# Optimization experiments

Hardware: AMD Instinct MI355X
Metric: run time of the kernel (lower is better)

## Reference

```python
import jax, jax.numpy as jnp
import numpy as np

# SplineConv (PyG), dim=1, kernel_size=2, degree=1, open spline, aggr='mean',
# root_weight=True, bias=True.
# For K=2, m=1, dim=1 the B-spline basis per edge reduces exactly to
#   basis = (1 - u, u) with kernel indices (0, 1), u = edge_attr[:, 0] in [0, 1].

N_NODES = 50000
N_EDGES = 1600000
D_IN = 128
D_OUT = 128


def setup_inputs() -> dict:
    key = jax.random.key(0)
    k1, k2, k3, k4, k5, k6, k7 = jax.random.split(key, 7)
    x = jax.random.normal(k1, (N_NODES, D_IN), dtype=jnp.float32)
    edge_index = jax.random.randint(k2, (2, N_EDGES), 0, N_NODES, dtype=jnp.int64)
    edge_attr = jax.random.uniform(k3, (N_EDGES, 1), dtype=jnp.float32)
    # Glorot-ish init for spline weights [K^dim=2, D_IN, D_OUT]
    scale = 1.0 / np.sqrt(D_IN)
    W = jax.random.normal(k4, (2, D_IN, D_OUT), dtype=jnp.float32) * scale
    W_root = jax.random.normal(k5, (D_IN, D_OUT), dtype=jnp.float32) * scale
    bias = jax.random.normal(k6, (D_OUT,), dtype=jnp.float32) * 0.01
    return {"x": x, "edge_index": edge_index, "edge_attr": edge_attr,
            "W": W, "W_root": W_root, "bias": bias}


def reference(x, edge_index, edge_attr, W, W_root, bias):
    n = x.shape[0]
    src, dst = edge_index[0], edge_index[1]
    u = jnp.clip(edge_attr[:, 0], 0.0, 1.0)          # [E]
    # Node-level GEMMs for both kernel weight slots (cheaper than per-edge GEMM)
    h = jnp.einsum('nd,kde->kne', x, W)              # [2, N, D_OUT]
    # Per-edge spline-weighted message: (1-u)*h0[src] + u*h1[src]
    msg = (1.0 - u)[:, None] * h[0][src] + u[:, None] * h[1][src]  # [E, D_OUT]
    agg = jax.ops.segment_sum(msg, dst, num_segments=n)            # [N, D_OUT]
    deg = jax.ops.segment_sum(jnp.ones_like(u), dst, num_segments=n)
    agg = agg / jnp.maximum(deg, 1.0)[:, None]       # mean aggregation
    return agg + x @ W_root + bias
```

## Files before the change

### kernel.cpp

```cpp
#include <hip/hip_runtime.h>

static constexpr int N = 50000;
static constexpr int E = 1600000;
static constexpr int D = 128;
static constexpr int NB = (N + 63) / 64;
static constexpr int BIN_BLKS = 256;
static constexpr int CHUNK = E / BIN_BLKS;
static constexpr int SLOTS = (CHUNK + 1023) / 1024;
static constexpr int BKT_CAP = 3072;
static constexpr int CVT_BLKS = (N * D / 8 + 1023) / 1024;
static constexpr int W_BLKS = 48;

typedef __attribute__((ext_vector_type(8))) short short8;
typedef __attribute__((ext_vector_type(4))) float f32x4;
typedef __attribute__((ext_vector_type(2))) float f32x2;

__device__ __forceinline__ uint bf16rne2(float a, float b) {
    uint ua = __float_as_uint(a), ub = __float_as_uint(b);
    ua += 0x7fffu + ((ua >> 16) & 1u);
    ub += 0x7fffu + ((ub >> 16) & 1u);
    return (ua >> 16) | (ub & 0xffff0000u);
}

__device__ __forceinline__ int logical_blk() {
    return (blockIdx.x & 7) * (BIN_BLKS / 8) + (blockIdx.x >> 3);
}

__global__ __launch_bounds__(1024) void binprep_k(
        const int* __restrict__ ei, const float* __restrict__ ea,
        const float* __restrict__ x, const float* __restrict__ W,
        const float* __restrict__ Wr, int* __restrict__ gcur,
        uint* __restrict__ pay, ushort* __restrict__ xb,
        uchar* __restrict__ xf8, ushort* __restrict__ Wt) {
    __shared__ int hist[NB];
    __shared__ int pfx[NB];
    __shared__ int base[NB];
    __shared__ uint srtpay[CHUNK];
    __shared__ int  srtpos[CHUNK];
    __shared__ int wsum[16];
    __shared__ int tot_s;
    int t = threadIdx.x;
    int lane = t & 63, wv = t >> 6;
    if (blockIdx.x < BIN_BLKS) {
        int b = logical_blk();
        if (t < NB) hist[t] = 0;
        __syncthreads();
        int b0 = b * CHUNK;
        uint mypay[SLOTS];
        int  mybkt[SLOTS];
        int  myrank[SLOTS];
#pragma unroll
        for (int k = 0; k < SLOTS; ++k) {
            int i = b0 + t + k * 1024;
            myrank[k] = -1;
            if (t + k * 1024 < CHUNK) {
                int dst = ei[E + i];
                if ((unsigned)dst < (unsigned)N) {
                    int src = ei[i];
                    float u = fminf(fmaxf(ea[i], 0.0f), 1.0f);
                    uint u10 = (uint)(u * 1023.0f + 0.5f);
                    int bkt = dst >> 6;
                    mybkt[k] = bkt;
                    mypay[k] = (u10 << 22) | ((uint)(dst & 63) << 16) | (uint)src;
                    myrank[k] = atomicAdd(&hist[bkt], 1);
                }
            }
        }
        __syncthreads();
        int c = (t < NB) ? hist[t] : 0;
        int s = c;
#pragma unroll
        for (int d = 1; d < 64; d <<= 1) {
            int o = __shfl_up(s, d);
            if (lane >= d) s += o;
        }
        if (lane == 63) wsum[wv] = s;
        __syncthreads();
        if (t < 16) {
            int v = wsum[t];
            int si = v;
#pragma unroll
            for (int d = 1; d < 16; d <<= 1) {
                int o = __shfl_up(si, d);
                if (t >= d) si += o;
            }
            wsum[t] = si - v;
            if (t == 15) tot_s = si;
        }
        __syncthreads();
        int excl = s - c + wsum[wv];
        if (t < NB) {
            pfx[t] = excl;
            base[t] = c ? atomicAdd(&gcur[t], c) : 0;
        }
        __syncthreads();
#pragma unroll
        for (int k = 0; k < SLOTS; ++k) {
            if (myrank[k] >= 0) {
                int bk = mybkt[k];
                int slot = pfx[bk] + myrank[k];
                srtpay[slot] = mypay[k];
                int p = base[bk] + myrank[k];
                srtpos[slot] = (p < BKT_CAP) ? (bk * BKT_CAP + p) : -1;
            }
        }
        __syncthreads();
        int tot = tot_s;
        for (int i = t; i < tot; i += 1024) {
            int pos = srtpos[i];
            if (pos >= 0) pay[pos] = srtpay[i];
        }
    } else if (blockIdx.x < BIN_BLKS + CVT_BLKS) {
        int i = (blockIdx.x - BIN_BLKS) * 1024 + t;
        if (i < N * D / 8) {
            float4 v0 = ((const float4*)x)[2 * i];
            float4 v1 = ((const float4*)x)[2 * i + 1];
            uint4 ob = { bf16rne2(v0.x, v0.y), bf16rne2(v0.z, v0.w),
                         bf16rne2(v1.x, v1.y), bf16rne2(v1.z, v1.w) };
            ((uint4*)xb)[i] = ob;
            int lo = __builtin_amdgcn_cvt_pk_fp8_f32(v0.x, v0.y, 0, false);
            lo = __builtin_amdgcn_cvt_pk_fp8_f32(v0.z, v0.w, lo, true);
            int hi = __builtin_amdgcn_cvt_pk_fp8_f32(v1.x, v1.y, 0, false);
            hi = __builtin_amdgcn_cvt_pk_fp8_f32(v1.z, v1.w, hi, true);
            uint2 o8 = { (uint)lo, (uint)hi };
            ((uint2*)xf8)[i] = o8;
        }
    } else {
        int i = (blockIdx.x - BIN_BLKS - CVT_BLKS) * 1024 + t;
        int n = i / 384, r = i % 384;
        float v = (r < 256) ? W[(size_t)r * 128 + n]
                            : Wr[(size_t)(r - 256) * 128 + n];
        uint u = __float_as_uint(v);
        u += 0x7fffu + ((u >> 16) & 1u);
        Wt[(size_t)n * 384 + r] = (ushort)(u >> 16);
    }
}

__global__ __launch_bounds__(1024) void sortagg_k(
        const uchar* __restrict__ xf8, const int* __restrict__ gcur,
        const uint* __restrict__ pay, ushort* __restrict__ a0b,
        ushort* __restrict__ a1b) {
    __shared__ uint srt[BKT_CAP];
    __shared__ int hist[64];
    __shared__ int off64[65];
    int b = blockIdx.x, t = threadIdx.x;
    int beg = b * BKT_CAP;
    int c = gcur[b];
    if (c > BKT_CAP) c = BKT_CAP;
    if (t < 64) hist[t] = 0;
    __syncthreads();
    uint mypay[3]; int myrank[3];
#pragma unroll
    for (int k = 0; k < 3; ++k) {
        int i = t + k * 1024;
        if (i < c) {
            uint p = pay[beg + i];
            mypay[k] = p;
            myrank[k] = atomicAdd(&hist[(p >> 16) & 63], 1);
        }
    }
    __syncthreads();
    if (t < 64) {
        int v = hist[t];
        int s = v;
        for (int d = 1; d < 64; d <<= 1) {
            int o = __shfl_up(s, d);
            if (t >= d) s += o;
        }
        off64[t] = s - v;
        if (t == 63) off64[64] = s;
    }
    __syncthreads();
#pragma unroll
    for (int k = 0; k < 3; ++k) {
        int i = t + k * 1024;
        if (i < c) {
            uint p = mypay[k];
            srt[off64[(p >> 16) & 63] + myrank[k]] = p;
        }
    }
    __syncthreads();

    int lane = t & 63;
    int wv   = t >> 6;
    int grp  = (lane >> 4);
    int cl   = lane & 15;
    int nloc = wv * 4 + grp;
    int s0 = off64[nloc], s1 = off64[nloc + 1];
    int deg = s1 - s0;

    f32x2 S[4], T[4];
#pragma unroll
    for (int q = 0; q < 4; ++q) { S[q] = 0.f; T[q] = 0.f; }

    int j = s0;
    for (; j + 3 < s1; j += 4) {
        uint p[4];
        uint2 v[4];
#pragma unroll
        for (int d = 0; d < 4; ++d) p[d] = srt[j + d];
#pragma unroll
        for (int d = 0; d < 4; ++d)
            v[d] = *(const uint2*)(xf8 + (size_t)(p[d] & 0xffffu) * D + cl * 8);
#pragma unroll
        for (int d = 0; d < 4; ++d) {
            float u = (float)(p[d] >> 22) * (1.0f / 1023.0f);
            f32x2 u2 = {u, u};
            f32x2 xv0 = __builtin_amdgcn_cvt_pk_f32_fp8((int)v[d].x, false);
            f32x2 xv1 = __builtin_amdgcn_cvt_pk_f32_fp8((int)v[d].x, true);
            f32x2 xv2 = __builtin_amdgcn_cvt_pk_f32_fp8((int)v[d].y, false);
            f32x2 xv3 = __builtin_amdgcn_cvt_pk_f32_fp8((int)v[d].y, true);
            S[0] += xv0; T[0] = u2 * xv0 + T[0];
            S[1] += xv1; T[1] = u2 * xv1 + T[1];
            S[2] += xv2; T[2] = u2 * xv2 + T[2];
            S[3] += xv3; T[3] = u2 * xv3 + T[3];
        }
    }
    for (; j < s1; ++j) {
        uint p0 = srt[j];
        uint2 v0 = *(const uint2*)(xf8 + (size_t)(p0 & 0xffffu) * D + cl * 8);
        float u = (float)(p0 >> 22) * (1.0f / 1023.0f);
        f32x2 u2 = {u, u};
        f32x2 xv0 = __builtin_amdgcn_cvt_pk_f32_fp8((int)v0.x, false);
        f32x2 xv1 = __builtin_amdgcn_cvt_pk_f32_fp8((int)v0.x, true);
        f32x2 xv2 = __builtin_amdgcn_cvt_pk_f32_fp8((int)v0.y, false);
        f32x2 xv3 = __builtin_amdgcn_cvt_pk_f32_fp8((int)v0.y, true);
        S[0] += xv0; T[0] = u2 * xv0 + T[0];
        S[1] += xv1; T[1] = u2 * xv1 + T[1];
        S[2] += xv2; T[2] = u2 * xv2 + T[2];
        S[3] += xv3; T[3] = u2 * xv3 + T[3];
    }

    int node = b * 64 + nloc;
    if (node < N) {
        float inv = 1.0f / fmaxf((float)deg, 1.0f);
        uint4 oa = { bf16rne2((S[0].x - T[0].x) * inv, (S[0].y - T[0].y) * inv),
                     bf16rne2((S[1].x - T[1].x) * inv, (S[1].y - T[1].y) * inv),
                     bf16rne2((S[2].x - T[2].x) * inv, (S[2].y - T[2].y) * inv),
                     bf16rne2((S[3].x - T[3].x) * inv, (S[3].y - T[3].y) * inv) };
        uint4 ob = { bf16rne2(T[0].x * inv, T[0].y * inv),
                     bf16rne2(T[1].x * inv, T[1].y * inv),
                     bf16rne2(T[2].x * inv, T[2].y * inv),
                     bf16rne2(T[3].x * inv, T[3].y * inv) };
        *(uint4*)(a0b + (size_t)node * D + cl * 8) = oa;
        *(uint4*)(a1b + (size_t)node * D + cl * 8) = ob;
    }
}

__global__ __launch_bounds__(256) void gemm_k(
        const ushort* __restrict__ a0b, const ushort* __restrict__ a1b,
        const ushort* __restrict__ xb, const ushort* __restrict__ Wt,
        const float* __restrict__ bias, float* __restrict__ out) {
    int t    = threadIdx.x;
    int lane = t & 63;
    int w    = t >> 6;
    int r2   = w >> 1, c2 = w & 1;
    int q    = lane >> 4;
    int l16  = lane & 15;
    int row0 = blockIdx.x * 128;

    f32x4 acc[4][4];
#pragma unroll
    for (int i = 0; i < 4; ++i)
#pragma unroll
        for (int j = 0; j < 4; ++j) acc[i][j] = 0.f;

    const ushort* Asrc[3] = {a0b, a1b, xb};

    int arow[4];
#pragma unroll
    for (int mt = 0; mt < 4; ++mt) {
        int r = row0 + r2 * 64 + mt * 16 + l16;
        arow[mt] = r < N ? r : N - 1;
    }

#pragma unroll
    for (int kt = 0; kt < 384; kt += 32) {
        const ushort* Ab = Asrc[kt >> 7];
        int ko = (kt & 127) + q * 8;
        short8 af[4], bf[4];
#pragma unroll
        for (int mt = 0; mt < 4; ++mt)
            af[mt] = *(const short8*)(Ab + (size_t)arow[mt] * 128 + ko);
#pragma unroll
        for (int nt = 0; nt < 4; ++nt) {
            int n = c2 * 64 + nt * 16 + l16;
            bf[nt] = *(const short8*)(Wt + (size_t)n * 384 + kt + q * 8);
        }
#pragma unroll
        for (int mt = 0; mt < 4; ++mt)
#pragma unroll
            for (int nt = 0; nt < 4; ++nt)
                acc[mt][nt] = __builtin_amdgcn_mfma_f32_16x16x32_bf16(
                    af[mt], bf[nt], acc[mt][nt], 0, 0, 0);
    }

#pragma unroll
    for (int nt = 0; nt < 4; ++nt) {
        int col = c2 * 64 + nt * 16 + l16;
        float bb = bias[col];
#pragma unroll
        for (int mt = 0; mt < 4; ++mt) {
#pragma unroll
            for (int r = 0; r < 4; ++r) {
                int row = row0 + r2 * 64 + mt * 16 + q * 4 + r;
                if (row < N) out[(size_t)row * 128 + col] = acc[mt][nt][r] + bb;
            }
        }
    }
}

extern "C" void kernel_launch(void* const* d_in, const int* in_sizes, int n_in,
                              void* d_out, int out_size, void* d_ws, size_t ws_size,
                              hipStream_t stream) {
    const float* x    = (const float*)d_in[0];
    const int*   ei   = (const int*)d_in[1];
    const float* ea   = (const float*)d_in[2];
    const float* W    = (const float*)d_in[3];
    const float* Wr   = (const float*)d_in[4];
    const float* bias = (const float*)d_in[5];
    float* out = (float*)d_out;

    char* ws = (char*)d_ws;
    size_t o = 0;
    auto alloc = [&](size_t bytes) -> void* {
        void* p = ws + o;
        o = (o + bytes + 255) & ~(size_t)255;
        return p;
    };
    int*    gcur = (int*)alloc((size_t)NB * 4);
    uint*   pay  = (uint*)alloc((size_t)NB * BKT_CAP * 4);
    ushort* xb   = (ushort*)alloc((size_t)N * D * 2);
    uchar*  xf8  = (uchar*)alloc((size_t)N * D);
    ushort* a0b  = (ushort*)alloc((size_t)N * D * 2);
    ushort* a1b  = (ushort*)alloc((size_t)N * D * 2);
    ushort* Wt   = (ushort*)alloc((size_t)128 * 384 * 2);
    (void)ws_size; (void)in_sizes; (void)n_in; (void)out_size;

    hipMemsetAsync(gcur, 0, (size_t)NB * 4, stream);
    binprep_k<<<BIN_BLKS + CVT_BLKS + W_BLKS, 1024, 0, stream>>>(
                 ei, ea, x, W, Wr, gcur, pay, xb, xf8, Wt);
    sortagg_k<<<NB, 1024, 0, stream>>>(xf8, gcur, pay, a0b, a1b);
    gemm_k   <<<(N + 127) / 128, 256, 0, stream>>>(a0b, a1b, xb, Wt, bias, out);
}
```

Measured before the change: 171.2 us.

## Stage GEMM A/B tiles in LDS via direct global-to-LDS loads with XOR swizzle

The final GEMM kernel now stages 128x64 tiles of A and B into shared memory using global_load_lds (direct global-to-LDS copies) with an XOR-swizzled layout, instead of each wave loading its MFMA operands straight from global memory. This is meant to cut redundant global/L2 traffic, since operands are now shared across the waves in a block, and to avoid LDS bank conflicts. In exchange it adds two barriers per K-step and has no double buffering, so load latency is not overlapped with compute. The GEMM is only a part of the total pipeline.

Measured after the change: 159.1 us. -7.1%, faster.

```diff
diff --git a/kernel.cpp b/kernel.cpp
--- a/kernel.cpp
+++ b/kernel.cpp
@@ -20,6 +20,12 @@
     ua += 0x7fffu + ((ua >> 16) & 1u);
     ub += 0x7fffu + ((ub >> 16) & 1u);
     return (ua >> 16) | (ub & 0xffff0000u);
+}
+
+__device__ __forceinline__ void gload16(const void* g, void* l) {
+    __builtin_amdgcn_global_load_lds(
+        (const __attribute__((address_space(1))) void*)g,
+        (__attribute__((address_space(3))) void*)l, 16, 0, 0);
 }
 
 __device__ __forceinline__ int logical_blk() {
@@ -251,6 +257,9 @@
         const ushort* __restrict__ a0b, const ushort* __restrict__ a1b,
         const ushort* __restrict__ xb, const ushort* __restrict__ Wt,
         const float* __restrict__ bias, float* __restrict__ out) {
+    __shared__ ushort As[128 * 64];
+    __shared__ ushort Bs[128 * 64];
+
     int t    = threadIdx.x;
     int lane = t & 63;
     int w    = t >> 6;
@@ -258,6 +267,9 @@
     int q    = lane >> 4;
     int l16  = lane & 15;
     int row0 = blockIdx.x * 128;
+    int rsub  = lane >> 3;
+    int cslot = lane & 7;
+    int xorc  = cslot ^ rsub;
 
     f32x4 acc[4][4];
 #pragma unroll
@@ -267,32 +279,42 @@
 
     const ushort* Asrc[3] = {a0b, a1b, xb};
 
-    int arow[4];
-#pragma unroll
-    for (int mt = 0; mt < 4; ++mt) {
-        int r = row0 + r2 * 64 + mt * 16 + l16;
-        arow[mt] = r < N ? r : N - 1;
-    }
-
-#pragma unroll
-    for (int kt = 0; kt < 384; kt += 32) {
+#pragma unroll
+    for (int kt = 0; kt < 384; kt += 64) {
         const ushort* Ab = Asrc[kt >> 7];
-        int ko = (kt & 127) + q * 8;
-        short8 af[4], bf[4];
-#pragma unroll
-        for (int mt = 0; mt < 4; ++mt)
-            af[mt] = *(const short8*)(Ab + (size_t)arow[mt] * 128 + ko);
-#pragma unroll
-        for (int nt = 0; nt < 4; ++nt) {
-            int n = c2 * 64 + nt * 16 + l16;
-            bf[nt] = *(const short8*)(Wt + (size_t)n * 384 + kt + q * 8);
-        }
-#pragma unroll
-        for (int mt = 0; mt < 4; ++mt)
-#pragma unroll
-            for (int nt = 0; nt < 4; ++nt)
-                acc[mt][nt] = __builtin_amdgcn_mfma_f32_16x16x32_bf16(
-                    af[mt], bf[nt], acc[mt][nt], 0, 0, 0);
+        int ko = kt & 127;
+#pragma unroll
+        for (int h = 0; h < 4; ++h) {
+            int region = h * 4 + w;
+            int r = region * 8 + rsub;
+            int ra = row0 + r; ra = ra < N ? ra : N - 1;
+            gload16(Ab + (size_t)ra * 128 + ko + xorc * 8, As + region * 512);
+            gload16(Wt + (size_t)r * 384 + kt + xorc * 8,  Bs + region * 512);
+        }
+        __syncthreads();
+#pragma unroll
+        for (int kk = 0; kk < 2; ++kk) {
+            short8 af[4], bf[4];
+#pragma unroll
+            for (int mt = 0; mt < 4; ++mt) {
+                int r = r2 * 64 + mt * 16 + l16;
+                int slot = (kk * 4 + q) ^ (r & 7);
+                af[mt] = *(const short8*)&As[r * 64 + slot * 8];
+            }
+#pragma unroll
+            for (int nt = 0; nt < 4; ++nt) {
+                int n = c2 * 64 + nt * 16 + l16;
+                int slot = (kk * 4 + q) ^ (n & 7);
+                bf[nt] = *(const short8*)&Bs[n * 64 + slot * 8];
+            }
+#pragma unroll
+            for (int mt = 0; mt < 4; ++mt)
+#pragma unroll
+                for (int nt = 0; nt < 4; ++nt)
+                    acc[mt][nt] = __builtin_amdgcn_mfma_f32_16x16x32_bf16(
+                        af[mt], bf[nt], acc[mt][nt], 0, 0, 0);
+        }
+        __syncthreads();
     }
 
 #pragma unroll
```

## Fuse aggregation and output GEMM into one kernel via shared-memory tiles

Applied to the files above, without the earlier changes.

Merges the sort/aggregate kernel with the GEMM kernel. Each 64-node block now writes its mean-aggregated bf16 rows into XOR-swizzled shared memory and then runs MFMA over them plus the x rows. This drops the global a0b/a1b intermediates and one kernel launch. In exchange each block adds 32KB of shared memory, which may lower occupancy, and uses a smaller per-wave GEMM tile with more redundant loads of Wt.

Result: slower. 192.3 us (+12.3%).

```diff
diff --git a/kernel.cpp b/kernel.cpp
--- a/kernel.cpp
+++ b/kernel.cpp
@@ -136,13 +136,16 @@
     }
 }
 
-__global__ __launch_bounds__(1024) void sortagg_k(
+__global__ __launch_bounds__(1024) void sortagggemm_k(
         const uchar* __restrict__ xf8, const int* __restrict__ gcur,
-        const uint* __restrict__ pay, ushort* __restrict__ a0b,
-        ushort* __restrict__ a1b) {
+        const uint* __restrict__ pay, const ushort* __restrict__ xb,
+        const ushort* __restrict__ Wt, const float* __restrict__ bias,
+        float* __restrict__ out) {
     __shared__ uint srt[BKT_CAP];
     __shared__ int hist[64];
     __shared__ int off64[65];
+    __shared__ ushort A0[64 * 128];
+    __shared__ ushort A1[64 * 128];
     int b = blockIdx.x, t = threadIdx.x;
     int beg = b * BKT_CAP;
     int c = gcur[b];
@@ -231,8 +234,7 @@
         S[3] += xv3; T[3] = u2 * xv3 + T[3];
     }
 
-    int node = b * 64 + nloc;
-    if (node < N) {
+    {
         float inv = 1.0f / fmaxf((float)deg, 1.0f);
         uint4 oa = { bf16rne2((S[0].x - T[0].x) * inv, (S[0].y - T[0].y) * inv),
                      bf16rne2((S[1].x - T[1].x) * inv, (S[1].y - T[1].y) * inv),
@@ -242,70 +244,46 @@
                      bf16rne2(T[1].x * inv, T[1].y * inv),
                      bf16rne2(T[2].x * inv, T[2].y * inv),
                      bf16rne2(T[3].x * inv, T[3].y * inv) };
-        *(uint4*)(a0b + (size_t)node * D + cl * 8) = oa;
-        *(uint4*)(a1b + (size_t)node * D + cl * 8) = ob;
-    }
-}
-
-__global__ __launch_bounds__(256) void gemm_k(
-        const ushort* __restrict__ a0b, const ushort* __restrict__ a1b,
-        const ushort* __restrict__ xb, const ushort* __restrict__ Wt,
-        const float* __restrict__ bias, float* __restrict__ out) {
-    int t    = threadIdx.x;
-    int lane = t & 63;
-    int w    = t >> 6;
-    int r2   = w >> 1, c2 = w & 1;
-    int q    = lane >> 4;
-    int l16  = lane & 15;
-    int row0 = blockIdx.x * 128;
-
-    f32x4 acc[4][4];
-#pragma unroll
-    for (int i = 0; i < 4; ++i)
-#pragma unroll
-        for (int j = 0; j < 4; ++j) acc[i][j] = 0.f;
-
-    const ushort* Asrc[3] = {a0b, a1b, xb};
-
-    int arow[4];
-#pragma unroll
-    for (int mt = 0; mt < 4; ++mt) {
-        int r = row0 + r2 * 64 + mt * 16 + l16;
-        arow[mt] = r < N ? r : N - 1;
-    }
-
-#pragma unroll
-    for (int kt = 0; kt < 384; kt += 32) {
-        const ushort* Ab = Asrc[kt >> 7];
-        int ko = (kt & 127) + q * 8;
-        short8 af[4], bf[4];
-#pragma unroll
-        for (int mt = 0; mt < 4; ++mt)
-            af[mt] = *(const short8*)(Ab + (size_t)arow[mt] * 128 + ko);
-#pragma unroll
-        for (int nt = 0; nt < 4; ++nt) {
-            int n = c2 * 64 + nt * 16 + l16;
-            bf[nt] = *(const short8*)(Wt + (size_t)n * 384 + kt + q * 8);
-        }
-#pragma unroll
-        for (int mt = 0; mt < 4; ++mt)
-#pragma unroll
-            for (int nt = 0; nt < 4; ++nt)
-                acc[mt][nt] = __builtin_amdgcn_mfma_f32_16x16x32_bf16(
-                    af[mt], bf[nt], acc[mt][nt], 0, 0, 0);
-    }
-
-#pragma unroll
-    for (int nt = 0; nt < 4; ++nt) {
-        int col = c2 * 64 + nt * 16 + l16;
-        float bb = bias[col];
-#pragma unroll
-        for (int mt = 0; mt < 4; ++mt) {
-#pragma unroll
-            for (int r = 0; r < 4; ++r) {
-                int row = row0 + r2 * 64 + mt * 16 + q * 4 + r;
-                if (row < N) out[(size_t)row * 128 + col] = acc[mt][nt][r] + bb;
-            }
+        int pc = cl ^ (nloc & 7);
+        *(uint4*)&A0[nloc * 128 + pc * 8] = oa;
+        *(uint4*)&A1[nloc * 128 + pc * 8] = ob;
+    }
+    __syncthreads();
+
+    int mt  = wv >> 2;
+    int nt0 = wv & 3, nt1 = nt0 + 4;
+    int q4  = lane >> 4;
+    int l16 = lane & 15;
+    int arow = mt * 16 + l16;
+    int rsw  = arow & 7;
+    int grow = b * 64 + arow;
+    const ushort* xrow = xb + (size_t)(grow < N ? grow : N - 1) * 128;
+
+    f32x4 acc0 = 0.f, acc1 = 0.f;
+#pragma unroll
+    for (int ks = 0; ks < 12; ++ks) {
+        int kt = ks * 32;
+        short8 af;
+        if (kt < 128)
+            af = *(const short8*)&A0[arow * 128 + ((((kt) >> 3) + q4) ^ rsw) * 8];
+        else if (kt < 256)
+            af = *(const short8*)&A1[arow * 128 + ((((kt - 128) >> 3) + q4) ^ rsw) * 8];
+        else
+            af = *(const short8*)(xrow + (kt - 256) + q4 * 8);
+        short8 bf0 = *(const short8*)(Wt + (size_t)(nt0 * 16 + l16) * 384 + kt + q4 * 8);
+        short8 bf1 = *(const short8*)(Wt + (size_t)(nt1 * 16 + l16) * 384 + kt + q4 * 8);
+        acc0 = __builtin_amdgcn_mfma_f32_16x16x32_bf16(af, bf0, acc0, 0, 0, 0);
+        acc1 = __builtin_amdgcn_mfma_f32_16x16x32_bf16(af, bf1, acc1, 0, 0, 0);
+    }
+
+    int orow = b * 64 + mt * 16 + q4 * 4;
+    float bb0 = bias[nt0 * 16 + l16];
+    float bb1 = bias[nt1 * 16 + l16];
+#pragma unroll
+    for (int r = 0; r < 4; ++r) {
+        if (orow + r < N) {
+            out[(size_t)(orow + r) * 128 + nt0 * 16 + l16] = acc0[r] + bb0;
+            out[(size_t)(orow + r) * 128 + nt1 * 16 + l16] = acc1[r] + bb1;
         }
     }
 }
@@ -332,14 +310,11 @@
     uint*   pay  = (uint*)alloc((size_t)NB * BKT_CAP * 4);
     ushort* xb   = (ushort*)alloc((size_t)N * D * 2);
     uchar*  xf8  = (uchar*)alloc((size_t)N * D);
-    ushort* a0b  = (ushort*)alloc((size_t)N * D * 2);
-    ushort* a1b  = (ushort*)alloc((size_t)N * D * 2);
     ushort* Wt   = (ushort*)alloc((size_t)128 * 384 * 2);
     (void)ws_size; (void)in_sizes; (void)n_in; (void)out_size;
 
     hipMemsetAsync(gcur, 0, (size_t)NB * 4, stream);
     binprep_k<<<BIN_BLKS + CVT_BLKS + W_BLKS, 1024, 0, stream>>>(
                  ei, ea, x, W, Wr, gcur, pay, xb, xf8, Wt);
-    sortagg_k<<<NB, 1024, 0, stream>>>(xf8, gcur, pay, a0b, a1b);
-    gemm_k   <<<(N + 127) / 128, 256, 0, stream>>>(a0b, a1b, xb, Wt, bias, out);
-}
+    sortagggemm_k<<<NB, 1024, 0, stream>>>(xf8, gcur, pay, xb, Wt, bias, out);
+}
```
